# Optimization experiments

Hardware: AMD Instinct MI355X
Metric: run time of the kernel (lower is better)

## Reference

```python
import jax, jax.numpy as jnp
import numpy as np

B, T, ENC, DEC, U = 64, 2048, 512, 512, 128

def setup_inputs() -> dict:
    key = jax.random.key(0)
    ks = jax.random.split(key, 8)
    s_dec = 1.0 / np.sqrt(DEC)
    s_enc = 1.0 / np.sqrt(ENC)
    s_u = 1.0 / np.sqrt(U)
    return {
        "decoder_hidden": jax.random.normal(ks[0], (B, DEC), jnp.float32),
        "encoder_outputs": jax.random.normal(ks[1], (B, T, ENC), jnp.float32),
        "Wa": jax.random.normal(ks[2], (DEC, U), jnp.float32) * s_dec,
        "ba": jnp.zeros((U,), jnp.float32),
        "Wb": jax.random.normal(ks[3], (ENC, U), jnp.float32) * s_enc,
        "bb": jnp.zeros((U,), jnp.float32),
        "Wv": jax.random.normal(ks[4], (U, 1), jnp.float32) * s_u,
        "bv": jnp.zeros((1,), jnp.float32),
    }

def reference(decoder_hidden, encoder_outputs, Wa, ba, Wb, bb, Wv, bv):
    # q: [B, 1, U] — decoder hidden projected, broadcast over time
    q = (decoder_hidden @ Wa + ba)[:, None, :]
    # k: [B, T, U]
    k = jnp.einsum('bte,eu->btu', encoder_outputs, Wb) + bb
    # score: [B, T, 1]
    score = jnp.tanh(q + k) @ Wv + bv
    attn = jax.nn.softmax(score, axis=1)          # [B, T, 1]
    context = jnp.sum(attn * encoder_outputs, axis=1)  # [B, ENC]
    return context, attn
```

## Files before the change

kernel.cpp:

```cpp
#include <hip/hip_runtime.h>
#include <math.h>

#define B_   64
#define T_   2048
#define ENC_ 512
#define U_   128
#define NC   16

typedef __attribute__((ext_vector_type(8))) short short8;
typedef __attribute__((ext_vector_type(4))) float float4v;

__device__ inline unsigned short bf16_rtn(float x) {
    unsigned u = __float_as_uint(x);
    unsigned r = u + 0x7FFFu + ((u >> 16) & 1u);
    return (unsigned short)(r >> 16);
}
__device__ inline float bf16_to_f32(unsigned short h) {
    return __uint_as_float(((unsigned)h) << 16);
}

__device__ inline void cvt_split8(const float4 a0, const float4 a1,
                                  short8& h, short8& l) {
    const float xs[8] = {a0.x, a0.y, a0.z, a0.w, a1.x, a1.y, a1.z, a1.w};
#pragma unroll
    for (int j = 0; j < 8; ++j) {
        const unsigned u  = __float_as_uint(xs[j]);
        const unsigned r  = u + 0x7FFFu + ((u >> 16) & 1u);
        const unsigned hb = r >> 16;
        h[j] = (short)hb;
        const float d = xs[j] - __uint_as_float(hb << 16);
        l[j] = (short)(__float_as_uint(d) >> 16);
    }
}

__device__ inline float fast_tanh(float x) {
    const float e = __expf(2.0f * x);
    return 1.0f - 2.0f / (e + 1.0f);
}

__global__ void qproj_kernel(const float* __restrict__ dh,
                             const float* __restrict__ Wa,
                             const float* __restrict__ ba,
                             const float* __restrict__ bb,
                             float* __restrict__ q) {
    const int b = blockIdx.x;
    const int u = threadIdx.x;
    const float* dhb = dh + b * ENC_;
    float a0 = 0.f, a1 = 0.f, a2 = 0.f, a3 = 0.f;
#pragma unroll 4
    for (int e = 0; e < ENC_; e += 4) {
        a0 += dhb[e + 0] * Wa[(e + 0) * U_ + u];
        a1 += dhb[e + 1] * Wa[(e + 1) * U_ + u];
        a2 += dhb[e + 2] * Wa[(e + 2) * U_ + u];
        a3 += dhb[e + 3] * Wa[(e + 3) * U_ + u];
    }
    q[b * U_ + u] = ((a0 + a1) + (a2 + a3)) + ba[u] + bb[u];
}

__global__ void wprep_kernel(const float* __restrict__ Wb,
                             unsigned short* __restrict__ whi,
                             unsigned short* __restrict__ wlo) {
    const int fid = blockIdx.x;
    const int c   = fid >> 3;
    const int gn  = fid & 7;
    const int L   = threadIdx.x;
    const int n   = gn * 16 + (L & 15);
    const int k0  = c * 32 + (L >> 4) * 8;
    short8 hi, lo;
#pragma unroll
    for (int j = 0; j < 8; ++j) {
        const float x = Wb[(size_t)(k0 + j) * U_ + n];
        const unsigned short h = bf16_rtn(x);
        hi[j] = (short)h;
        lo[j] = (short)bf16_rtn(x - bf16_to_f32(h));
    }
    *(short8*)(whi + ((size_t)fid * 64 + L) * 8) = hi;
    *(short8*)(wlo + ((size_t)fid * 64 + L) * 8) = lo;
}

__global__ void zero_kernel(float* __restrict__ p, int n) {
    const int i = blockIdx.x * 256 + threadIdx.x;
    if (i < n) p[i] = 0.f;
}

#define MBLK 128

__global__ __launch_bounds__(256, 2)
void score_ctx_kernel(const float* __restrict__ enc,
                      const unsigned short* __restrict__ whi,
                      const unsigned short* __restrict__ wlo,
                      const float* __restrict__ q,
                      const float* __restrict__ Wv,
                      float* __restrict__ expw,
                      float* __restrict__ uctx,
                      float* __restrict__ Zsum) {
    __shared__ __align__(16) short Ahi[2][4096];
    __shared__ __align__(16) short Alo[2][4096];
    __shared__ float ew[MBLK];

    const int tid = threadIdx.x;
    const int w   = tid >> 6;
    const int L   = tid & 63;
    const int m0  = blockIdx.x * MBLK;
    const int b   = m0 >> 11;

    const int srow = tid >> 2;
    const int sqd  = tid & 3;
    const int sf0  = ((srow >> 4) * 4 + sqd) * 16 + (srow & 15);
    const int sf1  = (((srow >> 4) + 4) * 4 + sqd) * 16 + (srow & 15);
    const float* encR0 = enc + (size_t)(m0 + srow) * ENC_ + sqd * 8;
    const float* encR1 = encR0 + (size_t)64 * ENC_;

    float4v acc0[8], acc1[8];
#pragma unroll
    for (int gn = 0; gn < 8; ++gn) { acc0[gn] = (float4v)0.f; acc1[gn] = (float4v)0.f; }

    {
        short8 h, l;
        cvt_split8(*(const float4*)(encR0), *(const float4*)(encR0 + 4), h, l);
        *(short8*)(&Ahi[0][sf0 * 8]) = h;
        *(short8*)(&Alo[0][sf0 * 8]) = l;
        cvt_split8(*(const float4*)(encR1), *(const float4*)(encR1 + 4), h, l);
        *(short8*)(&Ahi[0][sf1 * 8]) = h;
        *(short8*)(&Alo[0][sf1 * 8]) = l;
    }
    __syncthreads();

    for (int c = 0; c < NC; ++c) {
        const int cur = c & 1;
        float4 p00, p01, p10, p11;
        if (c < NC - 1) {
            p00 = *(const float4*)(encR0 + (c + 1) * 32);
            p01 = *(const float4*)(encR0 + (c + 1) * 32 + 4);
            p10 = *(const float4*)(encR1 + (c + 1) * 32);
            p11 = *(const float4*)(encR1 + (c + 1) * 32 + 4);
        }
        const short8 ah0 = *(const short8*)(&Ahi[cur][((2 * w + 0) * 64 + L) * 8]);
        const short8 al0 = *(const short8*)(&Alo[cur][((2 * w + 0) * 64 + L) * 8]);
        const short8 ah1 = *(const short8*)(&Ahi[cur][((2 * w + 1) * 64 + L) * 8]);
        const short8 al1 = *(const short8*)(&Alo[cur][((2 * w + 1) * 64 + L) * 8]);
        const unsigned short* bh_base = whi + ((size_t)(c * 8) * 64 + L) * 8;
        const unsigned short* bl_base = wlo + ((size_t)(c * 8) * 64 + L) * 8;
#pragma unroll
        for (int gn = 0; gn < 8; ++gn) {
            const short8 bh = *(const short8*)(bh_base + (size_t)gn * 512);
            const short8 bl = *(const short8*)(bl_base + (size_t)gn * 512);
            acc0[gn] = __builtin_amdgcn_mfma_f32_16x16x32_bf16(ah0, bh, acc0[gn], 0, 0, 0);
            acc0[gn] = __builtin_amdgcn_mfma_f32_16x16x32_bf16(ah0, bl, acc0[gn], 0, 0, 0);
            acc0[gn] = __builtin_amdgcn_mfma_f32_16x16x32_bf16(al0, bh, acc0[gn], 0, 0, 0);
            acc1[gn] = __builtin_amdgcn_mfma_f32_16x16x32_bf16(ah1, bh, acc1[gn], 0, 0, 0);
            acc1[gn] = __builtin_amdgcn_mfma_f32_16x16x32_bf16(ah1, bl, acc1[gn], 0, 0, 0);
            acc1[gn] = __builtin_amdgcn_mfma_f32_16x16x32_bf16(al1, bh, acc1[gn], 0, 0, 0);
        }
        if (c < NC - 1) {
            const int nxt = cur ^ 1;
            short8 h, l;
            cvt_split8(p00, p01, h, l);
            *(short8*)(&Ahi[nxt][sf0 * 8]) = h;
            *(short8*)(&Alo[nxt][sf0 * 8]) = l;
            cvt_split8(p10, p11, h, l);
            *(short8*)(&Ahi[nxt][sf1 * 8]) = h;
            *(short8*)(&Alo[nxt][sf1 * 8]) = l;
        }
        __syncthreads();
    }

    const int n15 = L & 15;
    float qv[8], wvv[8];
#pragma unroll
    for (int gn = 0; gn < 8; ++gn) {
        qv[gn]  = q[b * U_ + gn * 16 + n15];
        wvv[gn] = Wv[gn * 16 + n15];
    }
#pragma unroll
    for (int tt = 0; tt < 2; ++tt) {
        const float4v* accp = tt ? acc1 : acc0;
#pragma unroll
        for (int r = 0; r < 4; ++r) {
            float s = 0.f;
#pragma unroll
            for (int gn = 0; gn < 8; ++gn)
                s += fast_tanh(qv[gn] + accp[gn][r]) * wvv[gn];
            s += __shfl_xor(s, 1, 64);
            s += __shfl_xor(s, 2, 64);
            s += __shfl_xor(s, 4, 64);
            s += __shfl_xor(s, 8, 64);
            if (n15 == 0) {
                const int rloc = (2 * w + tt) * 16 + (L >> 4) * 4 + r;
                const float e = __expf(s);
                ew[rloc] = e;
                expw[m0 + rloc] = e;
            }
        }
    }
    __syncthreads();

    const int col = tid * 2;
    const float* ebase = enc + (size_t)m0 * ENC_ + col;
    float sx = 0.f, sy = 0.f;
#pragma unroll 8
    for (int t = 0; t < MBLK; ++t) {
        const float wgt = ew[t];
        const float2 v = *(const float2*)(ebase + (size_t)t * ENC_);
        sx += wgt * v.x;
        sy += wgt * v.y;
    }
    atomicAdd(&uctx[b * ENC_ + col], sx);
    atomicAdd(&uctx[b * ENC_ + col + 1], sy);

    if (tid < 64) {
        float z = ew[tid] + ew[tid + 64];
        z += __shfl_xor(z, 1, 64);
        z += __shfl_xor(z, 2, 64);
        z += __shfl_xor(z, 4, 64);
        z += __shfl_xor(z, 8, 64);
        z += __shfl_xor(z, 16, 64);
        z += __shfl_xor(z, 32, 64);
        if (tid == 0) atomicAdd(&Zsum[b], z);
    }
}

__global__ void normalize_kernel(const float* __restrict__ uctx,
                                 const float* __restrict__ Zsum,
                                 const float* __restrict__ expw,
                                 float* __restrict__ ctx,
                                 float* __restrict__ attn) {
    const int idx = blockIdx.x * 256 + threadIdx.x;
    if (idx < B_ * ENC_) {
        ctx[idx] = uctx[idx] / Zsum[idx >> 9];
    } else {
        const int i2 = idx - B_ * ENC_;
        attn[i2] = expw[i2] / Zsum[i2 >> 11];
    }
}

extern "C" void kernel_launch(void* const* d_in, const int* in_sizes, int n_in,
                              void* d_out, int out_size, void* d_ws, size_t ws_size,
                              hipStream_t stream) {
    const float* dh  = (const float*)d_in[0];
    const float* enc = (const float*)d_in[1];
    const float* Wa  = (const float*)d_in[2];
    const float* ba  = (const float*)d_in[3];
    const float* Wb  = (const float*)d_in[4];
    const float* bb  = (const float*)d_in[5];
    const float* Wv  = (const float*)d_in[6];

    float* out      = (float*)d_out;
    float* ctx      = out;
    float* attn_out = out + (B_ * ENC_);

    float* ws   = (float*)d_ws;
    float* q    = ws;
    float* expw = ws + 8192;
    float* uctx = ws + 8192 + B_ * T_;
    float* Zs   = uctx + B_ * ENC_;
    unsigned short* whi = (unsigned short*)(Zs + 64);
    unsigned short* wlo = whi + 65536;

    qproj_kernel<<<B_, U_, 0, stream>>>(dh, Wa, ba, bb, q);
    wprep_kernel<<<128, 64, 0, stream>>>(Wb, whi, wlo);
    zero_kernel<<<129, 256, 0, stream>>>(uctx, B_ * ENC_ + B_);
    score_ctx_kernel<<<(B_ * T_) / MBLK, 256, 0, stream>>>(enc, whi, wlo, q, Wv,
                                                           expw, uctx, Zs);
    normalize_kernel<<<(B_ * (ENC_ + T_)) / 256, 256, 0, stream>>>(uctx, Zs, expw,
                                                                   ctx, attn_out);
}
```

Measured before the change: 498.1 us.

## Stage Wb tiles in LDS and use a 2x2 warp tiling for the score GEMM

Previously each warp read the full Wb hi/lo fragments straight from global memory every chunk while covering all 128 U columns for 32 rows. Now the Wb chunk is cooperatively loaded into double-buffered shared memory next to the encoder tile, and warps are arranged 2x2 so each covers 64 rows and 64 columns, reusing A and B fragments across a 4x4 MFMA grid. Partial score sums from the two column halves are combined through an extra shared reduction and barrier before the exp. This roughly doubles LDS use and removes the occupancy hint from launch bounds, which may lower occupancy.

```diff
diff --git a/kernel.cpp b/kernel.cpp
--- a/kernel.cpp
+++ b/kernel.cpp
@@ -6,6 +6,7 @@
 #define ENC_ 512
 #define U_   128
 #define NC   16
+#define MBLK 128
 
 typedef __attribute__((ext_vector_type(8))) short short8;
 typedef __attribute__((ext_vector_type(4))) float float4v;
@@ -83,9 +84,7 @@
     if (i < n) p[i] = 0.f;
 }
 
-#define MBLK 128
-
-__global__ __launch_bounds__(256, 2)
+__global__ __launch_bounds__(256)
 void score_ctx_kernel(const float* __restrict__ enc,
                       const unsigned short* __restrict__ whi,
                       const unsigned short* __restrict__ wlo,
@@ -96,24 +95,31 @@
                       float* __restrict__ Zsum) {
     __shared__ __align__(16) short Ahi[2][4096];
     __shared__ __align__(16) short Alo[2][4096];
+    __shared__ __align__(16) short Bhi[2][4096];
+    __shared__ __align__(16) short Blo[2][4096];
+    __shared__ float sred[2 * MBLK];
     __shared__ float ew[MBLK];
 
     const int tid = threadIdx.x;
     const int w   = tid >> 6;
     const int L   = tid & 63;
+    const int wr  = w >> 1;
+    const int wc  = w & 1;
     const int m0  = blockIdx.x * MBLK;
     const int b   = m0 >> 11;
 
     const int srow = tid >> 2;
     const int sqd  = tid & 3;
     const int sf0  = ((srow >> 4) * 4 + sqd) * 16 + (srow & 15);
-    const int sf1  = (((srow >> 4) + 4) * 4 + sqd) * 16 + (srow & 15);
+    const int sf1  = sf0 + 256;
     const float* encR0 = enc + (size_t)(m0 + srow) * ENC_ + sqd * 8;
     const float* encR1 = encR0 + (size_t)64 * ENC_;
 
-    float4v acc0[8], acc1[8];
-#pragma unroll
-    for (int gn = 0; gn < 8; ++gn) { acc0[gn] = (float4v)0.f; acc1[gn] = (float4v)0.f; }
+    float4v acc[4][4];
+#pragma unroll
+    for (int mi = 0; mi < 4; ++mi)
+#pragma unroll
+        for (int gi = 0; gi < 4; ++gi) acc[mi][gi] = (float4v)0.f;
 
     {
         short8 h, l;
@@ -123,75 +129,103 @@
         cvt_split8(*(const float4*)(encR1), *(const float4*)(encR1 + 4), h, l);
         *(short8*)(&Ahi[0][sf1 * 8]) = h;
         *(short8*)(&Alo[0][sf1 * 8]) = l;
+        *(short8*)(&Bhi[0][tid * 16])     = *(const short8*)(whi + tid * 16);
+        *(short8*)(&Bhi[0][tid * 16 + 8]) = *(const short8*)(whi + tid * 16 + 8);
+        *(short8*)(&Blo[0][tid * 16])     = *(const short8*)(wlo + tid * 16);
+        *(short8*)(&Blo[0][tid * 16 + 8]) = *(const short8*)(wlo + tid * 16 + 8);
     }
     __syncthreads();
 
     for (int c = 0; c < NC; ++c) {
         const int cur = c & 1;
-        float4 p00, p01, p10, p11;
+        float4 pa0, pa1, pa2, pa3;
+        short8 pbh0, pbh1, pbl0, pbl1;
         if (c < NC - 1) {
-            p00 = *(const float4*)(encR0 + (c + 1) * 32);
-            p01 = *(const float4*)(encR0 + (c + 1) * 32 + 4);
-            p10 = *(const float4*)(encR1 + (c + 1) * 32);
-            p11 = *(const float4*)(encR1 + (c + 1) * 32 + 4);
-        }
-        const short8 ah0 = *(const short8*)(&Ahi[cur][((2 * w + 0) * 64 + L) * 8]);
-        const short8 al0 = *(const short8*)(&Alo[cur][((2 * w + 0) * 64 + L) * 8]);
-        const short8 ah1 = *(const short8*)(&Ahi[cur][((2 * w + 1) * 64 + L) * 8]);
-        const short8 al1 = *(const short8*)(&Alo[cur][((2 * w + 1) * 64 + L) * 8]);
-        const unsigned short* bh_base = whi + ((size_t)(c * 8) * 64 + L) * 8;
-        const unsigned short* bl_base = wlo + ((size_t)(c * 8) * 64 + L) * 8;
-#pragma unroll
-        for (int gn = 0; gn < 8; ++gn) {
-            const short8 bh = *(const short8*)(bh_base + (size_t)gn * 512);
-            const short8 bl = *(const short8*)(bl_base + (size_t)gn * 512);
-            acc0[gn] = __builtin_amdgcn_mfma_f32_16x16x32_bf16(ah0, bh, acc0[gn], 0, 0, 0);
-            acc0[gn] = __builtin_amdgcn_mfma_f32_16x16x32_bf16(ah0, bl, acc0[gn], 0, 0, 0);
-            acc0[gn] = __builtin_amdgcn_mfma_f32_16x16x32_bf16(al0, bh, acc0[gn], 0, 0, 0);
-            acc1[gn] = __builtin_amdgcn_mfma_f32_16x16x32_bf16(ah1, bh, acc1[gn], 0, 0, 0);
-            acc1[gn] = __builtin_amdgcn_mfma_f32_16x16x32_bf16(ah1, bl, acc1[gn], 0, 0, 0);
-            acc1[gn] = __builtin_amdgcn_mfma_f32_16x16x32_bf16(al1, bh, acc1[gn], 0, 0, 0);
-        }
+            pa0 = *(const float4*)(encR0 + (c + 1) * 32);
+            pa1 = *(const float4*)(encR0 + (c + 1) * 32 + 4);
+            pa2 = *(const float4*)(encR1 + (c + 1) * 32);
+            pa3 = *(const float4*)(encR1 + (c + 1) * 32 + 4);
+            const unsigned short* bh = whi + (size_t)(c + 1) * 4096 + tid * 16;
+            const unsigned short* bl = wlo + (size_t)(c + 1) * 4096 + tid * 16;
+            pbh0 = *(const short8*)(bh);
+            pbh1 = *(const short8*)(bh + 8);
+            pbl0 = *(const short8*)(bl);
+            pbl1 = *(const short8*)(bl + 8);
+        }
+
+        short8 ah[4], al[4], bh[4], bl[4];
+#pragma unroll
+        for (int mi = 0; mi < 4; ++mi) {
+            const int mt = wr * 4 + mi;
+            ah[mi] = *(const short8*)(&Ahi[cur][(mt * 64 + L) * 8]);
+            al[mi] = *(const short8*)(&Alo[cur][(mt * 64 + L) * 8]);
+        }
+#pragma unroll
+        for (int gi = 0; gi < 4; ++gi) {
+            const int gt = wc * 4 + gi;
+            bh[gi] = *(const short8*)(&Bhi[cur][(gt * 64 + L) * 8]);
+            bl[gi] = *(const short8*)(&Blo[cur][(gt * 64 + L) * 8]);
+        }
+
+#pragma unroll
+        for (int mi = 0; mi < 4; ++mi)
+#pragma unroll
+            for (int gi = 0; gi < 4; ++gi) {
+                acc[mi][gi] = __builtin_amdgcn_mfma_f32_16x16x32_bf16(ah[mi], bh[gi], acc[mi][gi], 0, 0, 0);
+                acc[mi][gi] = __builtin_amdgcn_mfma_f32_16x16x32_bf16(ah[mi], bl[gi], acc[mi][gi], 0, 0, 0);
+                acc[mi][gi] = __builtin_amdgcn_mfma_f32_16x16x32_bf16(al[mi], bh[gi], acc[mi][gi], 0, 0, 0);
+            }
+
         if (c < NC - 1) {
             const int nxt = cur ^ 1;
             short8 h, l;
-            cvt_split8(p00, p01, h, l);
+            cvt_split8(pa0, pa1, h, l);
             *(short8*)(&Ahi[nxt][sf0 * 8]) = h;
             *(short8*)(&Alo[nxt][sf0 * 8]) = l;
-            cvt_split8(p10, p11, h, l);
+            cvt_split8(pa2, pa3, h, l);
             *(short8*)(&Ahi[nxt][sf1 * 8]) = h;
             *(short8*)(&Alo[nxt][sf1 * 8]) = l;
+            *(short8*)(&Bhi[nxt][tid * 16])     = pbh0;
+            *(short8*)(&Bhi[nxt][tid * 16 + 8]) = pbh1;
+            *(short8*)(&Blo[nxt][tid * 16])     = pbl0;
+            *(short8*)(&Blo[nxt][tid * 16 + 8]) = pbl1;
         }
         __syncthreads();
     }
 
     const int n15 = L & 15;
-    float qv[8], wvv[8];
-#pragma unroll
-    for (int gn = 0; gn < 8; ++gn) {
-        qv[gn]  = q[b * U_ + gn * 16 + n15];
-        wvv[gn] = Wv[gn * 16 + n15];
-    }
-#pragma unroll
-    for (int tt = 0; tt < 2; ++tt) {
-        const float4v* accp = tt ? acc1 : acc0;
+    float qv[4], wvv[4];
+#pragma unroll
+    for (int gi = 0; gi < 4; ++gi) {
+        const int u = wc * 64 + gi * 16 + n15;
+        qv[gi]  = q[b * U_ + u];
+        wvv[gi] = Wv[u];
+    }
+#pragma unroll
+    for (int mi = 0; mi < 4; ++mi) {
 #pragma unroll
         for (int r = 0; r < 4; ++r) {
             float s = 0.f;
 #pragma unroll
-            for (int gn = 0; gn < 8; ++gn)
-                s += fast_tanh(qv[gn] + accp[gn][r]) * wvv[gn];
+            for (int gi = 0; gi < 4; ++gi)
+                s += fast_tanh(qv[gi] + acc[mi][gi][r]) * wvv[gi];
             s += __shfl_xor(s, 1, 64);
             s += __shfl_xor(s, 2, 64);
             s += __shfl_xor(s, 4, 64);
             s += __shfl_xor(s, 8, 64);
             if (n15 == 0) {
-                const int rloc = (2 * w + tt) * 16 + (L >> 4) * 4 + r;
-                const float e = __expf(s);
-                ew[rloc] = e;
-                expw[m0 + rloc] = e;
+                const int mrow = wr * 64 + mi * 16 + (L >> 4) * 4 + r;
+                sred[wc * MBLK + mrow] = s;
             }
         }
+    }
+    __syncthreads();
+
+    if (tid < MBLK) {
+        const float s = sred[tid] + sred[MBLK + tid];
+        const float e = __expf(s);
+        ew[tid] = e;
+        expw[m0 + tid] = e;
     }
     __syncthreads();
 
```

Result: faster. 433.6 us (-13.0%).
